# Kernel tuning notes

Measured on AMD Instinct MI355X. Metric: run time of the kernel, lower is better.

Reference implementation:

```python
import jax, jax.numpy as jnp
import numpy as np

N, D, L = 200000, 256, 4  # nodes, feature dim, num_levels


def _l2norm(x, eps=1e-12):
    # matches F.normalize(p=2, dim=-1): x / max(||x||, eps)
    n = jnp.linalg.norm(x, axis=-1, keepdims=True)
    return x / jnp.clip(n, eps)


def setup_inputs() -> dict:
    key = jax.random.key(0)
    ks = jax.random.split(key, 6)
    inp = {}
    for i in range(4):
        inp[f"x{i}"] = jax.random.normal(ks[i], (N, D), dtype=jnp.float32)
    # nn.Linear(2*dim, 1): weight [1, 2D] stored here as vector [2D], bias [1]
    bound = 1.0 / float(np.sqrt(2 * D))
    inp["w_att"] = jax.random.uniform(ks[4], (2 * D,), jnp.float32, -bound, bound)
    inp["b_att"] = jax.random.uniform(ks[5], (1,), jnp.float32, -bound, bound)
    return inp


def reference(x0, x1, x2, x3, w_att, b_att):
    # ATT branch, eval mode (dropout is identity at inference)
    d = x0.shape[-1]
    query_n = _l2norm(x0)                       # [N, D]
    msgs = _l2norm(jnp.stack([x1, x2, x3]))     # [L-1, N, D], normalized messages
    # lin_att(cat((message, query), -1)) == message @ w_m + query @ w_q + b
    w_m, w_q = w_att[:d], w_att[d:]
    score = (jnp.einsum('lnd,d->ln', msgs, w_m)
             + query_n @ w_q + b_att[0])        # [L-1, N]
    score = jax.nn.leaky_relu(score, negative_slope=0.01)
    # segment softmax over index[1] = range(N)*(L-1): exactly softmax over level axis
    score = jax.nn.softmax(score, axis=0)       # [L-1, N]
    # scatter-add of score * message per node == weighted sum over levels
    embedding = x0 + jnp.einsum('ln,lnd->nd', score, msgs)  # [N, D]
    # flatten score to match cat-order of message rows ([x1 rows; x2 rows; x3 rows])
    return embedding, score.reshape(-1)
```

## Files before the change

kernel.cpp:

```cpp
#include <hip/hip_runtime.h>

#define D 256
#define F4_PER_ROW (D / 4)

typedef float fx4 __attribute__((ext_vector_type(4)));

__device__ __forceinline__ float dot4(float4 a, float4 b) {
    return fmaf(a.x, b.x, fmaf(a.y, b.y, fmaf(a.z, b.z, a.w * b.w)));
}

__device__ __forceinline__ void nt_store4(float4 v, float4* p) {
    fx4 t; t.x = v.x; t.y = v.y; t.z = v.z; t.w = v.w;
    __builtin_nontemporal_store(t, reinterpret_cast<fx4*>(p));
}

__global__ __launch_bounds__(256) void merge_xs_kernel(
    const float* __restrict__ x0, const float* __restrict__ x1,
    const float* __restrict__ x2, const float* __restrict__ x3,
    const float* __restrict__ w_att, const float* __restrict__ b_att,
    float* __restrict__ emb, float* __restrict__ sc_out, int N)
{
    const int lane = threadIdx.x & 63;
    const int sub  = lane & 31;
    const int half = lane >> 5;
    const int wid  = threadIdx.x >> 6;
    const int wpb  = blockDim.x >> 6;

    const int nUnits = (N + 1) >> 1;
    const int unit = blockIdx.x * wpb + wid;
    if (unit >= nUnits) return;

    const int row = unit * 2 + half;
    const bool valid = row < N;
    const size_t base = valid ? ((size_t)row * F4_PER_ROW + sub) : (size_t)sub;

    const float4* x0f = reinterpret_cast<const float4*>(x0);
    const float4* x1f = reinterpret_cast<const float4*>(x1);
    const float4* x2f = reinterpret_cast<const float4*>(x2);
    const float4* x3f = reinterpret_cast<const float4*>(x3);
    float4* embf      = reinterpret_cast<float4*>(emb);

    float4 v0a = x0f[base], v0b = x0f[base + 32];
    float4 v1a = x1f[base], v1b = x1f[base + 32];
    float4 v2a = x2f[base], v2b = x2f[base + 32];
    float4 v3a = x3f[base], v3b = x3f[base + 32];

    const float4* wmf = reinterpret_cast<const float4*>(w_att);
    const float4* wqf = wmf + 64;
    const float4 wma = wmf[sub], wmb = wmf[sub + 32];
    const float4 wqa = wqf[sub], wqb = wqf[sub + 32];
    const float b = b_att[0];

    float r0 = dot4(v0a, v0a) + dot4(v0b, v0b);
    float r1 = dot4(v0a, wqa) + dot4(v0b, wqb);
    float r2 = dot4(v1a, v1a) + dot4(v1b, v1b);
    float r3 = dot4(v1a, wma) + dot4(v1b, wmb);
    float r4 = dot4(v2a, v2a) + dot4(v2b, v2b);
    float r5 = dot4(v2a, wma) + dot4(v2b, wmb);
    float r6 = dot4(v3a, v3a) + dot4(v3b, v3b);
    float r7 = dot4(v3a, wma) + dot4(v3b, wmb);

    #pragma unroll
    for (int off = 16; off > 0; off >>= 1) {
        r0 += __shfl_xor(r0, off, 64);
        r1 += __shfl_xor(r1, off, 64);
        r2 += __shfl_xor(r2, off, 64);
        r3 += __shfl_xor(r3, off, 64);
        r4 += __shfl_xor(r4, off, 64);
        r5 += __shfl_xor(r5, off, 64);
        r6 += __shfl_xor(r6, off, 64);
        r7 += __shfl_xor(r7, off, 64);
    }

    const float n0 = fmaxf(sqrtf(r0), 1e-12f);
    const float n1 = fmaxf(sqrtf(r2), 1e-12f);
    const float n2 = fmaxf(sqrtf(r4), 1e-12f);
    const float n3 = fmaxf(sqrtf(r6), 1e-12f);

    const float qterm = r1 / n0 + b;
    float s1 = r3 / n1 + qterm;
    float s2 = r5 / n2 + qterm;
    float s3 = r7 / n3 + qterm;

    s1 = s1 > 0.f ? s1 : 0.01f * s1;
    s2 = s2 > 0.f ? s2 : 0.01f * s2;
    s3 = s3 > 0.f ? s3 : 0.01f * s3;

    const float m  = fmaxf(s1, fmaxf(s2, s3));
    const float e1 = expf(s1 - m);
    const float e2 = expf(s2 - m);
    const float e3 = expf(s3 - m);
    const float inv = 1.0f / (e1 + e2 + e3);
    const float sc1 = e1 * inv, sc2 = e2 * inv, sc3 = e3 * inv;

    const float c1 = sc1 / n1, c2 = sc2 / n2, c3 = sc3 / n3;
    float4 oa, ob;
    oa.x = fmaf(c1, v1a.x, fmaf(c2, v2a.x, fmaf(c3, v3a.x, v0a.x)));
    oa.y = fmaf(c1, v1a.y, fmaf(c2, v2a.y, fmaf(c3, v3a.y, v0a.y)));
    oa.z = fmaf(c1, v1a.z, fmaf(c2, v2a.z, fmaf(c3, v3a.z, v0a.z)));
    oa.w = fmaf(c1, v1a.w, fmaf(c2, v2a.w, fmaf(c3, v3a.w, v0a.w)));
    ob.x = fmaf(c1, v1b.x, fmaf(c2, v2b.x, fmaf(c3, v3b.x, v0b.x)));
    ob.y = fmaf(c1, v1b.y, fmaf(c2, v2b.y, fmaf(c3, v3b.y, v0b.y)));
    ob.z = fmaf(c1, v1b.z, fmaf(c2, v2b.z, fmaf(c3, v3b.z, v0b.z)));
    ob.w = fmaf(c1, v1b.w, fmaf(c2, v2b.w, fmaf(c3, v3b.w, v0b.w)));

    if (valid) {
        nt_store4(oa, &embf[base]);
        nt_store4(ob, &embf[base + 32]);
        if (sub == 0) {
            __builtin_nontemporal_store(sc1, &sc_out[row]);
            __builtin_nontemporal_store(sc2, &sc_out[N + row]);
            __builtin_nontemporal_store(sc3, &sc_out[2 * N + row]);
        }
    }
}

extern "C" void kernel_launch(void* const* d_in, const int* in_sizes, int n_in,
                              void* d_out, int out_size, void* d_ws, size_t ws_size,
                              hipStream_t stream) {
    const float* x0    = (const float*)d_in[0];
    const float* x1    = (const float*)d_in[1];
    const float* x2    = (const float*)d_in[2];
    const float* x3    = (const float*)d_in[3];
    const float* w_att = (const float*)d_in[4];
    const float* b_att = (const float*)d_in[5];

    const int N = in_sizes[0] / D;
    float* emb = (float*)d_out;
    float* sc  = emb + (size_t)N * D;

    const int threads = 256;
    const int wpb = threads / 64;
    const int nUnits = (N + 1) / 2;
    const int blocks = (nUnits + wpb - 1) / wpb;

    merge_xs_kernel<<<blocks, threads, 0, stream>>>(x0, x1, x2, x3, w_att, b_att,
                                                    emb, sc, N);
}
```

Measured before the change: 185.9 us.

## Convert to grid-stride loop with register prefetch of next row pair

Each wave now processes about eight row-pair units in a grid-stride loop. Before computing the current unit, it issues the global loads for the next unit into a second set of registers, so load latency overlaps with the reductions, softmax and stores. The launch grid shrinks to match. This doubles the live vector registers per thread, which may lower occupancy. It also drops the clamped base index, so a half-wave whose row equals N when N is odd would read out of bounds.

```diff
diff --git a/kernel.cpp b/kernel.cpp
--- a/kernel.cpp
+++ b/kernel.cpp
@@ -25,14 +25,11 @@
     const int half = lane >> 5;
     const int wid  = threadIdx.x >> 6;
     const int wpb  = blockDim.x >> 6;
+    const int nwaves = gridDim.x * wpb;
 
     const int nUnits = (N + 1) >> 1;
-    const int unit = blockIdx.x * wpb + wid;
+    int unit = blockIdx.x * wpb + wid;
     if (unit >= nUnits) return;
-
-    const int row = unit * 2 + half;
-    const bool valid = row < N;
-    const size_t base = valid ? ((size_t)row * F4_PER_ROW + sub) : (size_t)sub;
 
     const float4* x0f = reinterpret_cast<const float4*>(x0);
     const float4* x1f = reinterpret_cast<const float4*>(x1);
@@ -40,78 +37,101 @@
     const float4* x3f = reinterpret_cast<const float4*>(x3);
     float4* embf      = reinterpret_cast<float4*>(emb);
 
-    float4 v0a = x0f[base], v0b = x0f[base + 32];
-    float4 v1a = x1f[base], v1b = x1f[base + 32];
-    float4 v2a = x2f[base], v2b = x2f[base + 32];
-    float4 v3a = x3f[base], v3b = x3f[base + 32];
-
     const float4* wmf = reinterpret_cast<const float4*>(w_att);
     const float4* wqf = wmf + 64;
     const float4 wma = wmf[sub], wmb = wmf[sub + 32];
     const float4 wqa = wqf[sub], wqb = wqf[sub + 32];
     const float b = b_att[0];
 
-    float r0 = dot4(v0a, v0a) + dot4(v0b, v0b);
-    float r1 = dot4(v0a, wqa) + dot4(v0b, wqb);
-    float r2 = dot4(v1a, v1a) + dot4(v1b, v1b);
-    float r3 = dot4(v1a, wma) + dot4(v1b, wmb);
-    float r4 = dot4(v2a, v2a) + dot4(v2b, v2b);
-    float r5 = dot4(v2a, wma) + dot4(v2b, wmb);
-    float r6 = dot4(v3a, v3a) + dot4(v3b, v3b);
-    float r7 = dot4(v3a, wma) + dot4(v3b, wmb);
+    size_t base = (size_t)(unit * 2 + half) * F4_PER_ROW + sub;
+    float4 v0a = x0f[base], v0b = x0f[base + 32];
+    float4 v1a = x1f[base], v1b = x1f[base + 32];
+    float4 v2a = x2f[base], v2b = x2f[base + 32];
+    float4 v3a = x3f[base], v3b = x3f[base + 32];
 
-    #pragma unroll
-    for (int off = 16; off > 0; off >>= 1) {
-        r0 += __shfl_xor(r0, off, 64);
-        r1 += __shfl_xor(r1, off, 64);
-        r2 += __shfl_xor(r2, off, 64);
-        r3 += __shfl_xor(r3, off, 64);
-        r4 += __shfl_xor(r4, off, 64);
-        r5 += __shfl_xor(r5, off, 64);
-        r6 += __shfl_xor(r6, off, 64);
-        r7 += __shfl_xor(r7, off, 64);
-    }
+    for (;;) {
+        const int next = unit + nwaves;
+        const bool has_next = next < nUnits;
 
-    const float n0 = fmaxf(sqrtf(r0), 1e-12f);
-    const float n1 = fmaxf(sqrtf(r2), 1e-12f);
-    const float n2 = fmaxf(sqrtf(r4), 1e-12f);
-    const float n3 = fmaxf(sqrtf(r6), 1e-12f);
+        float4 p0a, p0b, p1a, p1b, p2a, p2b, p3a, p3b;
+        size_t nbase = 0;
+        if (has_next) {
+            nbase = (size_t)(next * 2 + half) * F4_PER_ROW + sub;
+            p0a = x0f[nbase]; p0b = x0f[nbase + 32];
+            p1a = x1f[nbase]; p1b = x1f[nbase + 32];
+            p2a = x2f[nbase]; p2b = x2f[nbase + 32];
+            p3a = x3f[nbase]; p3b = x3f[nbase + 32];
+        }
 
-    const float qterm = r1 / n0 + b;
-    float s1 = r3 / n1 + qterm;
-    float s2 = r5 / n2 + qterm;
-    float s3 = r7 / n3 + qterm;
+        float r0 = dot4(v0a, v0a) + dot4(v0b, v0b);
+        float r1 = dot4(v0a, wqa) + dot4(v0b, wqb);
+        float r2 = dot4(v1a, v1a) + dot4(v1b, v1b);
+        float r3 = dot4(v1a, wma) + dot4(v1b, wmb);
+        float r4 = dot4(v2a, v2a) + dot4(v2b, v2b);
+        float r5 = dot4(v2a, wma) + dot4(v2b, wmb);
+        float r6 = dot4(v3a, v3a) + dot4(v3b, v3b);
+        float r7 = dot4(v3a, wma) + dot4(v3b, wmb);
 
-    s1 = s1 > 0.f ? s1 : 0.01f * s1;
-    s2 = s2 > 0.f ? s2 : 0.01f * s2;
-    s3 = s3 > 0.f ? s3 : 0.01f * s3;
+        #pragma unroll
+        for (int off = 16; off > 0; off >>= 1) {
+            r0 += __shfl_xor(r0, off, 64);
+            r1 += __shfl_xor(r1, off, 64);
+            r2 += __shfl_xor(r2, off, 64);
+            r3 += __shfl_xor(r3, off, 64);
+            r4 += __shfl_xor(r4, off, 64);
+            r5 += __shfl_xor(r5, off, 64);
+            r6 += __shfl_xor(r6, off, 64);
+            r7 += __shfl_xor(r7, off, 64);
+        }
 
-    const float m  = fmaxf(s1, fmaxf(s2, s3));
-    const float e1 = expf(s1 - m);
-    const float e2 = expf(s2 - m);
-    const float e3 = expf(s3 - m);
-    const float inv = 1.0f / (e1 + e2 + e3);
-    const float sc1 = e1 * inv, sc2 = e2 * inv, sc3 = e3 * inv;
+        const float n0 = fmaxf(sqrtf(r0), 1e-12f);
+        const float n1 = fmaxf(sqrtf(r2), 1e-12f);
+        const float n2 = fmaxf(sqrtf(r4), 1e-12f);
+        const float n3 = fmaxf(sqrtf(r6), 1e-12f);
 
-    const float c1 = sc1 / n1, c2 = sc2 / n2, c3 = sc3 / n3;
-    float4 oa, ob;
-    oa.x = fmaf(c1, v1a.x, fmaf(c2, v2a.x, fmaf(c3, v3a.x, v0a.x)));
-    oa.y = fmaf(c1, v1a.y, fmaf(c2, v2a.y, fmaf(c3, v3a.y, v0a.y)));
-    oa.z = fmaf(c1, v1a.z, fmaf(c2, v2a.z, fmaf(c3, v3a.z, v0a.z)));
-    oa.w = fmaf(c1, v1a.w, fmaf(c2, v2a.w, fmaf(c3, v3a.w, v0a.w)));
-    ob.x = fmaf(c1, v1b.x, fmaf(c2, v2b.x, fmaf(c3, v3b.x, v0b.x)));
-    ob.y = fmaf(c1, v1b.y, fmaf(c2, v2b.y, fmaf(c3, v3b.y, v0b.y)));
-    ob.z = fmaf(c1, v1b.z, fmaf(c2, v2b.z, fmaf(c3, v3b.z, v0b.z)));
-    ob.w = fmaf(c1, v1b.w, fmaf(c2, v2b.w, fmaf(c3, v3b.w, v0b.w)));
+        const float qterm = r1 / n0 + b;
+        float s1 = r3 / n1 + qterm;
+        float s2 = r5 / n2 + qterm;
+        float s3 = r7 / n3 + qterm;
 
-    if (valid) {
-        nt_store4(oa, &embf[base]);
-        nt_store4(ob, &embf[base + 32]);
-        if (sub == 0) {
-            __builtin_nontemporal_store(sc1, &sc_out[row]);
-            __builtin_nontemporal_store(sc2, &sc_out[N + row]);
-            __builtin_nontemporal_store(sc3, &sc_out[2 * N + row]);
+        s1 = s1 > 0.f ? s1 : 0.01f * s1;
+        s2 = s2 > 0.f ? s2 : 0.01f * s2;
+        s3 = s3 > 0.f ? s3 : 0.01f * s3;
+
+        const float m  = fmaxf(s1, fmaxf(s2, s3));
+        const float e1 = expf(s1 - m);
+        const float e2 = expf(s2 - m);
+        const float e3 = expf(s3 - m);
+        const float inv = 1.0f / (e1 + e2 + e3);
+        const float sc1 = e1 * inv, sc2 = e2 * inv, sc3 = e3 * inv;
+
+        const float c1 = sc1 / n1, c2 = sc2 / n2, c3 = sc3 / n3;
+        float4 oa, ob;
+        oa.x = fmaf(c1, v1a.x, fmaf(c2, v2a.x, fmaf(c3, v3a.x, v0a.x)));
+        oa.y = fmaf(c1, v1a.y, fmaf(c2, v2a.y, fmaf(c3, v3a.y, v0a.y)));
+        oa.z = fmaf(c1, v1a.z, fmaf(c2, v2a.z, fmaf(c3, v3a.z, v0a.z)));
+        oa.w = fmaf(c1, v1a.w, fmaf(c2, v2a.w, fmaf(c3, v3a.w, v0a.w)));
+        ob.x = fmaf(c1, v1b.x, fmaf(c2, v2b.x, fmaf(c3, v3b.x, v0b.x)));
+        ob.y = fmaf(c1, v1b.y, fmaf(c2, v2b.y, fmaf(c3, v3b.y, v0b.y)));
+        ob.z = fmaf(c1, v1b.z, fmaf(c2, v2b.z, fmaf(c3, v3b.z, v0b.z)));
+        ob.w = fmaf(c1, v1b.w, fmaf(c2, v2b.w, fmaf(c3, v3b.w, v0b.w)));
+
+        const int row = unit * 2 + half;
+        if (row < N) {
+            nt_store4(oa, &embf[base]);
+            nt_store4(ob, &embf[base + 32]);
+            if (sub == 0) {
+                __builtin_nontemporal_store(sc1, &sc_out[row]);
+                __builtin_nontemporal_store(sc2, &sc_out[N + row]);
+                __builtin_nontemporal_store(sc3, &sc_out[2 * N + row]);
+            }
         }
+
+        if (!has_next) break;
+        v0a = p0a; v0b = p0b; v1a = p1a; v1b = p1b;
+        v2a = p2a; v2b = p2b; v3a = p3a; v3b = p3b;
+        base = nbase;
+        unit = next;
     }
 }
 
@@ -132,8 +152,9 @@
     const int threads = 256;
     const int wpb = threads / 64;
     const int nUnits = (N + 1) / 2;
-    const int blocks = (nUnits + wpb - 1) / wpb;
-
+    const int ITERS = 8;
+    int nwaves = (nUnits + ITERS - 1) / ITERS;
+    int blocks = (nwaves + wpb - 1) / wpb;
     merge_xs_kernel<<<blocks, threads, 0, stream>>>(x0, x1, x2, x3, w_att, b_att,
                                                     emb, sc, N);
 }
```

Result: slower. 209.6 us (+12.7%).
